# Performance work log

Hardware: AMD Instinct MI355X
Metric: run time of the kernel (lower is better)

The kernel has to match this reference:

```python
import jax, jax.numpy as jnp
import numpy as np

EPS = 1e-9  # Dice BatchNormalization epsilon


def dice(x, alpha):
    # Keras BatchNormalization(axis=-1, center=False, scale=False) in training
    # mode: normalize over all axes except the last using batch statistics.
    mean = jnp.mean(x, axis=(0, 1), keepdims=True)
    var = jnp.var(x, axis=(0, 1), keepdims=True)
    x_normed = (x - mean) * jax.lax.rsqrt(var + EPS)
    p = jax.nn.sigmoid(x_normed)
    return alpha * (1.0 - p) * x + p * x


def setup_inputs() -> dict:
    key = jax.random.key(0)
    ks = jax.random.split(key, 11)
    B, T, D = 512, 2048, 20
    keys_ = jax.random.normal(ks[0], (B, T, D), dtype=jnp.float32)
    query = jax.random.normal(ks[1], (B, 1, D), dtype=jnp.float32)
    mask = jax.random.randint(ks[2], (B, T), 0, 2) > 0
    # DNN tower weights: hidden dims 80 -> 32 -> 16, attention head 16 -> 1
    W0 = jax.random.normal(ks[3], (80, 32), dtype=jnp.float32) * 0.1
    b0 = jax.random.normal(ks[4], (32,), dtype=jnp.float32) * 0.1
    a0 = jax.random.normal(ks[5], (32,), dtype=jnp.float32) * 0.1
    W1 = jax.random.normal(ks[6], (32, 16), dtype=jnp.float32) * 0.1
    b1 = jax.random.normal(ks[7], (16,), dtype=jnp.float32) * 0.1
    a1 = jax.random.normal(ks[8], (16,), dtype=jnp.float32) * 0.1
    wk = jax.random.normal(ks[9], (16, 1), dtype=jnp.float32) * 0.1
    bk = jax.random.normal(ks[10], (1,), dtype=jnp.float32) * 0.1
    return {"keys": keys_, "query": query, "mask": mask,
            "W0": W0, "b0": b0, "a0": a0,
            "W1": W1, "b1": b1, "a1": a1,
            "wk": wk, "bk": bk}


def reference(keys, query, mask, W0, b0, a0, W1, b1, a1, wk, bk):
    B, T, D = keys.shape
    # repeat query along the key/time axis: [B,1,D] -> [B,T,D]
    queries = jnp.broadcast_to(query, (B, T, D))
    # local-activation features: [B,T,4D] = [B,T,80]
    att = jnp.concatenate([queries, keys, queries - keys, queries * keys], axis=-1)
    # DNN tower with Dice activations (dropout is identity at inference)
    h = dice(att @ W0 + b0, a0)   # [B,T,32]
    h = dice(h @ W1 + b1, a1)     # [B,T,16]
    score = h @ wk + bk           # [B,T,1]
    outputs = jnp.transpose(score, (0, 2, 1))  # [B,1,T]
    # NOTE: the original code computes the masked scores into self.outputs but
    # then (weight_normalization=False, return_score=False) overwrites it with
    # matmul(outputs, keys) using the UNMASKED scores -- we reproduce that.
    return jnp.matmul(outputs, keys)  # [B,1,D]
```

## Files before the change

### kernel.cpp

```cpp
#include <hip/hip_runtime.h>


#define BB 512
#define TT 2048
#define DD 20
#define C0 32
#define C1 16

#define NTH 256
#define NPOS 4
#define POSB (NTH * NPOS)

#define WS_SUM0 0
#define WS_SQ0 32
#define WS_SUM1 64
#define WS_SQ1 80
#define WS_BLOB 192
#define BLOB_J 24
#define BLOB_B (C0 * BLOB_J)
#define EPS 1e-9f

#define PIN(x) asm volatile("" : "+v"(x))

__device__ __forceinline__ float fast_sigmoid(float x) {
    return __builtin_amdgcn_rcpf(1.0f + __expf(-x));
}

__device__ __forceinline__ void load_krow(const float* __restrict__ row,
                                          float* kk) {
    const float4* kr = (const float4*)row;
    float4 a = kr[0], b = kr[1], c = kr[2], d = kr[3], e = kr[4];
    kk[0] = a.x; kk[1] = a.y; kk[2] = a.z; kk[3] = a.w;
    kk[4] = b.x; kk[5] = b.y; kk[6] = b.z; kk[7] = b.w;
    kk[8] = c.x; kk[9] = c.y; kk[10] = c.z; kk[11] = c.w;
    kk[12] = d.x; kk[13] = d.y; kk[14] = d.z; kk[15] = d.w;
    kk[16] = e.x; kk[17] = e.y; kk[18] = e.z; kk[19] = e.w;
}

__global__ void prep_kernel(const float* __restrict__ query,
                            const float* __restrict__ W0,
                            const float* __restrict__ b0,
                            float* __restrict__ blob) {
    const int b = blockIdx.x * 2 + (threadIdx.x >> 5);
    const int j = threadIdx.x & 31;
    float cj = b0[j];
    float* dst = blob + (size_t)b * BLOB_B + j * BLOB_J;
#pragma unroll
    for (int d = 0; d < DD; ++d) {
        float w_q = W0[d * C0 + j];
        float w_k = W0[(DD + d) * C0 + j];
        float w_d = W0[(2 * DD + d) * C0 + j];
        float w_p = W0[(3 * DD + d) * C0 + j];
        float qd = query[b * DD + d];
        dst[d] = w_k - w_d + qd * w_p;
        cj = fmaf(qd, w_q + w_d, cj);
    }
    dst[20] = cj;
}

__global__ __launch_bounds__(NTH, 2) void pass1_kernel(
    const float* __restrict__ keys, const float* __restrict__ blob,
    float* __restrict__ ws) {
    const int b = blockIdx.x >> 2, chunk = blockIdx.x & 3;
    const int tid = threadIdx.x, wave = tid >> 6, lane = tid & 63;
    const float* kbase = keys + ((size_t)b * TT + chunk * (TT / 4)) * DD;
    const float* wb = blob + (size_t)b * BLOB_B;

    float kk[2][DD];
    load_krow(kbase + (size_t)tid * DD, kk[0]);
    load_krow(kbase + (size_t)(tid + NTH) * DD, kk[1]);
#pragma unroll
    for (int pp = 0; pp < 2; ++pp)
#pragma unroll
        for (int d = 0; d < DD; ++d) PIN(kk[pp][d]);

    float s[C0], q[C0];
#pragma unroll
    for (int j = 0; j < C0; ++j) { s[j] = 0.f; q[j] = 0.f; }

#pragma unroll
    for (int j = 0; j < C0; ++j) {
        const float* w = wb + j * BLOB_J;
        float h0 = w[20], h1v = w[20];
#pragma unroll
        for (int d = 0; d < DD; ++d) {
            h0 = fmaf(kk[0][d], w[d], h0);
            h1v = fmaf(kk[1][d], w[d], h1v);
        }
        s[j] += h0 + h1v;
        q[j] = fmaf(h0, h0, q[j]);
        q[j] = fmaf(h1v, h1v, q[j]);
    }
    float mine = 0.f;
#pragma unroll
    for (int v = 0; v < 64; ++v) {
        float val = (v < C0) ? s[v] : q[v - C0];
#pragma unroll
        for (int o = 32; o >= 1; o >>= 1) val += __shfl_xor(val, o);
        if (lane == v) mine = val;
    }
    __shared__ float red[4][64];
    red[wave][lane] = mine;
    __syncthreads();
    if (tid < 64)
        atomicAdd(&ws[tid],
                  red[0][tid] + red[1][tid] + red[2][tid] + red[3][tid]);
}

#define LOAD_AND_PIN_KEYS()                                                  \
    const float* kbase = keys + ((size_t)b * TT + chunk * POSB) * DD;        \
    float kk[NPOS][DD];                                                      \
    _Pragma("unroll") for (int pp = 0; pp < NPOS; ++pp)                      \
        load_krow(kbase + (size_t)(tid + pp * NTH) * DD, kk[pp]);            \
    _Pragma("unroll") for (int pp = 0; pp < NPOS; ++pp)                      \
        _Pragma("unroll") for (int d = 0; d < DD; ++d) PIN(kk[pp][d]);

#define TOWER_JLOOP()                                                        \
    _Pragma("unroll 2") for (int j = 0; j < C0; ++j) {                       \
        float4 P = ld0[j];            \
        const float* w = wb + j * BLOB_J;             \
        const float* u = W1 + j * C1;                 \
        float h[NPOS];                                                       \
        _Pragma("unroll") for (int pp = 0; pp < NPOS; ++pp) {                \
            float hh = P.x;                                                  \
            _Pragma("unroll") for (int d = 0; d < DD; ++d)                   \
                hh = fmaf(kk[pp][d], w[d], hh);                              \
            h[pp] = hh;                                                      \
        }                                                                    \
        _Pragma("unroll") for (int pp = 0; pp < NPOS; ++pp) {                \
            float pr = fast_sigmoid(fmaf(h[pp], P.y, P.z));                  \
            float h0d = h[pp] * (P.w + pr * (1.0f - P.w));                   \
            _Pragma("unroll") for (int c = 0; c < C1; ++c)                   \
                h1[pp][c] = fmaf(h0d, u[c], h1[pp][c]);                      \
        }                                                                    \
    }

#define STAGE_DICE0()                                                        \
    if (tid < C0) {                                                          \
        const float invN = 1.0f / (float)(BB * TT);                          \
        float mean = ws[WS_SUM0 + tid] * invN;                               \
        float ex2 = ws[WS_SQ0 + tid] * invN;                                 \
        float sc = rsqrtf(ex2 - mean * mean + EPS);                          \
        ld0[tid] = make_float4(blob[(size_t)b * BLOB_B + tid * BLOB_J + 20], \
                               sc, -mean * sc, a0[tid]);                     \
    }

__global__ __launch_bounds__(NTH, 2) void pass2_kernel(
    const float* __restrict__ keys, const float* __restrict__ blob,
    const float* __restrict__ a0, const float* __restrict__ W1,
    const float* __restrict__ b1, float* __restrict__ ws) {
    const int b = blockIdx.x >> 1, chunk = blockIdx.x & 1;
    const int tid = threadIdx.x, wave = tid >> 6, lane = tid & 63;
    const float* wb = blob + (size_t)b * BLOB_B;
    __shared__ float4 ld0[C0];
    __shared__ float red[4][32];
    STAGE_DICE0()
    __syncthreads();

    LOAD_AND_PIN_KEYS()

    float h1[NPOS][C1];
#pragma unroll
    for (int pp = 0; pp < NPOS; ++pp)
#pragma unroll
        for (int c = 0; c < C1; ++c) h1[pp][c] = 0.f;

    TOWER_JLOOP()

    float s1[C1], q1[C1];
#pragma unroll
    for (int c = 0; c < C1; ++c) {
        float bc = b1[c], sv = 0.f, qv = 0.f;
#pragma unroll
        for (int pp = 0; pp < NPOS; ++pp) {
            float v = h1[pp][c] + bc;
            sv += v;
            qv = fmaf(v, v, qv);
        }
        s1[c] = sv;
        q1[c] = qv;
    }
    float mine = 0.f;
#pragma unroll
    for (int v = 0; v < 32; ++v) {
        float val = (v < C1) ? s1[v] : q1[v - C1];
#pragma unroll
        for (int o = 32; o >= 1; o >>= 1) val += __shfl_xor(val, o);
        if (lane == v) mine = val;
    }
    if (lane < 32) red[wave][lane] = mine;
    __syncthreads();
    if (tid < 32)
        atomicAdd(&ws[WS_SUM1 + tid],
                  red[0][tid] + red[1][tid] + red[2][tid] + red[3][tid]);
}

__global__ __launch_bounds__(NTH, 2) void pass3_kernel(
    const float* __restrict__ keys, const float* __restrict__ blob,
    const float* __restrict__ a0, const float* __restrict__ W1,
    const float* __restrict__ b1, const float* __restrict__ a1,
    const float* __restrict__ wk, const float* __restrict__ bk,
    const float* __restrict__ ws, float* __restrict__ out) {
    const int b = blockIdx.x >> 1, chunk = blockIdx.x & 1;
    const int tid = threadIdx.x, wave = tid >> 6, lane = tid & 63;
    const float* wb = blob + (size_t)b * BLOB_B;
    __shared__ float4 ld0[C0];
    __shared__ float4 ld1[C1];
    __shared__ float red[4][DD];
    STAGE_DICE0()
    if (tid < C1) {
        const float invN = 1.0f / (float)(BB * TT);
        float mean = ws[WS_SUM1 + tid] * invN;
        float ex2 = ws[WS_SQ1 + tid] * invN;
        float sc = rsqrtf(ex2 - mean * mean + EPS);
        ld1[tid] = make_float4(sc, -mean * sc, a1[tid], wk[tid]);
    }
    __syncthreads();

    LOAD_AND_PIN_KEYS()

    float h1[NPOS][C1];
#pragma unroll
    for (int pp = 0; pp < NPOS; ++pp)
#pragma unroll
        for (int c = 0; c < C1; ++c) h1[pp][c] = 0.f;

    TOWER_JLOOP()

    const float bkv = bk[0];
    float oacc[DD];
#pragma unroll
    for (int d = 0; d < DD; ++d) oacc[d] = 0.f;
#pragma unroll
    for (int pp = 0; pp < NPOS; ++pp) {
        float score = bkv;
#pragma unroll
        for (int c = 0; c < C1; ++c) {
            float v = h1[pp][c] + b1[c];
            float4 Q = ld1[c];
            float pr = fast_sigmoid(fmaf(v, Q.x, Q.y));
            float hd = v * (Q.z + pr * (1.0f - Q.z));
            score = fmaf(hd, Q.w, score);
        }
#pragma unroll
        for (int d = 0; d < DD; ++d) oacc[d] = fmaf(score, kk[pp][d], oacc[d]);
    }
    float mine = 0.f;
#pragma unroll
    for (int v = 0; v < DD; ++v) {
        float val = oacc[v];
#pragma unroll
        for (int o = 32; o >= 1; o >>= 1) val += __shfl_xor(val, o);
        if (lane == v) mine = val;
    }
    if (lane < DD) red[wave][lane] = mine;
    __syncthreads();
    if (tid < DD)
        atomicAdd(&out[b * DD + tid],
                  red[0][tid] + red[1][tid] + red[2][tid] + red[3][tid]);
}

extern "C" void kernel_launch(void* const* d_in, const int* in_sizes, int n_in,
                              void* d_out, int out_size, void* d_ws,
                              size_t ws_size, hipStream_t stream) {
    const float* keys = (const float*)d_in[0];
    const float* query = (const float*)d_in[1];
    const float* W0 = (const float*)d_in[3];
    const float* b0 = (const float*)d_in[4];
    const float* a0 = (const float*)d_in[5];
    const float* W1 = (const float*)d_in[6];
    const float* b1 = (const float*)d_in[7];
    const float* a1 = (const float*)d_in[8];
    const float* wk = (const float*)d_in[9];
    const float* bk = (const float*)d_in[10];
    float* out = (float*)d_out;
    float* ws = (float*)d_ws;
    float* blob = ws + WS_BLOB;

    hipMemsetAsync(ws, 0, 96 * sizeof(float), stream);
    hipMemsetAsync(out, 0, (size_t)out_size * sizeof(float), stream);

    prep_kernel<<<BB / 2, 64, 0, stream>>>(query, W0, b0, blob);

    pass1_kernel<<<BB * 4, NTH, 0, stream>>>(keys, blob, ws);
    pass2_kernel<<<BB * 2, NTH, 0, stream>>>(keys, blob, a0, W1, b1, ws);
    pass3_kernel<<<BB * 2, NTH, 0, stream>>>(keys, blob, a0, W1, b1, a1, wk,
                                             bk, ws, out);
}
```

Before: 298.5 us.

## Use reduce-scatter warp reductions, loop pass1 per batch, fully unroll tower

Replaces the per-value butterfly reductions (one full xor-shuffle tree per output value) with a reduce-scatter pattern that halves the live values at each shuffle stage, cutting the shuffle count in all three passes. Pass1 now launches one block per batch row and loops over the T axis in 4-row chunks instead of four blocks each handling two rows per thread, so each block does fewer atomics but the grid has fewer, longer blocks. The tower j-loop is fully unrolled and the Dice blend is rewritten as an fma. The trade-off is higher register pressure from the 64-entry value arrays and full unrolling, plus lower parallelism in pass1.

```diff
diff --git a/kernel.cpp b/kernel.cpp
--- a/kernel.cpp
+++ b/kernel.cpp
@@ -37,6 +37,36 @@
     kk[16] = e.x; kk[17] = e.y; kk[18] = e.z; kk[19] = e.w;
 }
 
+__device__ __forceinline__ float reduce_scatter_64(float* vals, int lane) {
+#pragma unroll
+    for (int m = 32; m >= 1; m >>= 1) {
+        bool hi = (lane & m) != 0;
+#pragma unroll
+        for (int i = 0; i < m; ++i) {
+            float keep = hi ? vals[m + i] : vals[i];
+            float send = hi ? vals[i] : vals[m + i];
+            vals[i] = keep + __shfl_xor(send, m);
+        }
+    }
+    return vals[0];
+}
+
+__device__ __forceinline__ float reduce_scatter_32(float* vals, int lane) {
+#pragma unroll
+    for (int i = 0; i < 32; ++i) vals[i] += __shfl_xor(vals[i], 32);
+#pragma unroll
+    for (int m = 16; m >= 1; m >>= 1) {
+        bool hi = (lane & m) != 0;
+#pragma unroll
+        for (int i = 0; i < m; ++i) {
+            float keep = hi ? vals[m + i] : vals[i];
+            float send = hi ? vals[i] : vals[m + i];
+            vals[i] = keep + __shfl_xor(send, m);
+        }
+    }
+    return vals[0];
+}
+
 __global__ void prep_kernel(const float* __restrict__ query,
                             const float* __restrict__ W0,
                             const float* __restrict__ b0,
@@ -61,46 +91,50 @@
 __global__ __launch_bounds__(NTH, 2) void pass1_kernel(
     const float* __restrict__ keys, const float* __restrict__ blob,
     float* __restrict__ ws) {
-    const int b = blockIdx.x >> 2, chunk = blockIdx.x & 3;
+    const int b = blockIdx.x;
     const int tid = threadIdx.x, wave = tid >> 6, lane = tid & 63;
-    const float* kbase = keys + ((size_t)b * TT + chunk * (TT / 4)) * DD;
+    const float* kbase = keys + (size_t)b * TT * DD;
     const float* wb = blob + (size_t)b * BLOB_B;
 
-    float kk[2][DD];
-    load_krow(kbase + (size_t)tid * DD, kk[0]);
-    load_krow(kbase + (size_t)(tid + NTH) * DD, kk[1]);
-#pragma unroll
-    for (int pp = 0; pp < 2; ++pp)
-#pragma unroll
-        for (int d = 0; d < DD; ++d) PIN(kk[pp][d]);
-
     float s[C0], q[C0];
 #pragma unroll
     for (int j = 0; j < C0; ++j) { s[j] = 0.f; q[j] = 0.f; }
 
-#pragma unroll
-    for (int j = 0; j < C0; ++j) {
-        const float* w = wb + j * BLOB_J;
-        float h0 = w[20], h1v = w[20];
-#pragma unroll
-        for (int d = 0; d < DD; ++d) {
-            h0 = fmaf(kk[0][d], w[d], h0);
-            h1v = fmaf(kk[1][d], w[d], h1v);
-        }
-        s[j] += h0 + h1v;
-        q[j] = fmaf(h0, h0, q[j]);
-        q[j] = fmaf(h1v, h1v, q[j]);
-    }
-    float mine = 0.f;
-#pragma unroll
-    for (int v = 0; v < 64; ++v) {
-        float val = (v < C0) ? s[v] : q[v - C0];
-#pragma unroll
-        for (int o = 32; o >= 1; o >>= 1) val += __shfl_xor(val, o);
-        if (lane == v) mine = val;
-    }
+#pragma unroll 1
+    for (int it = 0; it < TT / POSB; ++it) {
+        float kk[NPOS][DD];
+#pragma unroll
+        for (int pp = 0; pp < NPOS; ++pp)
+            load_krow(kbase + (size_t)(it * POSB + pp * NTH + tid) * DD,
+                      kk[pp]);
+#pragma unroll
+        for (int pp = 0; pp < NPOS; ++pp)
+#pragma unroll
+            for (int d = 0; d < DD; ++d) PIN(kk[pp][d]);
+
+#pragma unroll
+        for (int j = 0; j < C0; ++j) {
+            const float* w = wb + j * BLOB_J;
+            float h[NPOS];
+#pragma unroll
+            for (int pp = 0; pp < NPOS; ++pp) {
+                float hh = w[20];
+#pragma unroll
+                for (int d = 0; d < DD; ++d) hh = fmaf(kk[pp][d], w[d], hh);
+                h[pp] = hh;
+            }
+            s[j] += (h[0] + h[1]) + (h[2] + h[3]);
+#pragma unroll
+            for (int pp = 0; pp < NPOS; ++pp) q[j] = fmaf(h[pp], h[pp], q[j]);
+        }
+    }
+
+    float vals[64];
+#pragma unroll
+    for (int v = 0; v < 64; ++v) vals[v] = (v < C0) ? s[v] : q[v - C0];
+    float tot = reduce_scatter_64(vals, lane);
     __shared__ float red[4][64];
-    red[wave][lane] = mine;
+    red[wave][lane] = tot;
     __syncthreads();
     if (tid < 64)
         atomicAdd(&ws[tid],
@@ -116,7 +150,7 @@
         _Pragma("unroll") for (int d = 0; d < DD; ++d) PIN(kk[pp][d]);
 
 #define TOWER_JLOOP()                                                        \
-    _Pragma("unroll 2") for (int j = 0; j < C0; ++j) {                       \
+    _Pragma("unroll") for (int j = 0; j < C0; ++j) {                         \
         float4 P = ld0[j];            \
         const float* w = wb + j * BLOB_J;             \
         const float* u = W1 + j * C1;                 \
@@ -127,9 +161,10 @@
                 hh = fmaf(kk[pp][d], w[d], hh);                              \
             h[pp] = hh;                                                      \
         }                                                                    \
+        float oml = 1.0f - P.w;                                              \
         _Pragma("unroll") for (int pp = 0; pp < NPOS; ++pp) {                \
             float pr = fast_sigmoid(fmaf(h[pp], P.y, P.z));                  \
-            float h0d = h[pp] * (P.w + pr * (1.0f - P.w));                   \
+            float h0d = h[pp] * fmaf(pr, oml, P.w);                          \
             _Pragma("unroll") for (int c = 0; c < C1; ++c)                   \
                 h1[pp][c] = fmaf(h0d, u[c], h1[pp][c]);                      \
         }                                                                    \
@@ -167,7 +202,7 @@
 
     TOWER_JLOOP()
 
-    float s1[C1], q1[C1];
+    float vals[32];
 #pragma unroll
     for (int c = 0; c < C1; ++c) {
         float bc = b1[c], sv = 0.f, qv = 0.f;
@@ -177,18 +212,11 @@
             sv += v;
             qv = fmaf(v, v, qv);
         }
-        s1[c] = sv;
-        q1[c] = qv;
-    }
-    float mine = 0.f;
-#pragma unroll
-    for (int v = 0; v < 32; ++v) {
-        float val = (v < C1) ? s1[v] : q1[v - C1];
-#pragma unroll
-        for (int o = 32; o >= 1; o >>= 1) val += __shfl_xor(val, o);
-        if (lane == v) mine = val;
-    }
-    if (lane < 32) red[wave][lane] = mine;
+        vals[c] = sv;
+        vals[C1 + c] = qv;
+    }
+    float tot = reduce_scatter_32(vals, lane);
+    if (lane < 32) red[wave][lane] = tot;
     __syncthreads();
     if (tid < 32)
         atomicAdd(&ws[WS_SUM1 + tid],
@@ -206,7 +234,7 @@
     const float* wb = blob + (size_t)b * BLOB_B;
     __shared__ float4 ld0[C0];
     __shared__ float4 ld1[C1];
-    __shared__ float red[4][DD];
+    __shared__ float red[4][32];
     STAGE_DICE0()
     if (tid < C1) {
         const float invN = 1.0f / (float)(BB * TT);
@@ -239,21 +267,17 @@
             float v = h1[pp][c] + b1[c];
             float4 Q = ld1[c];
             float pr = fast_sigmoid(fmaf(v, Q.x, Q.y));
-            float hd = v * (Q.z + pr * (1.0f - Q.z));
+            float hd = v * fmaf(pr, 1.0f - Q.z, Q.z);
             score = fmaf(hd, Q.w, score);
         }
 #pragma unroll
         for (int d = 0; d < DD; ++d) oacc[d] = fmaf(score, kk[pp][d], oacc[d]);
     }
-    float mine = 0.f;
-#pragma unroll
-    for (int v = 0; v < DD; ++v) {
-        float val = oacc[v];
-#pragma unroll
-        for (int o = 32; o >= 1; o >>= 1) val += __shfl_xor(val, o);
-        if (lane == v) mine = val;
-    }
-    if (lane < DD) red[wave][lane] = mine;
+    float vals[32];
+#pragma unroll
+    for (int v = 0; v < 32; ++v) vals[v] = (v < DD) ? oacc[v] : 0.f;
+    float tot = reduce_scatter_32(vals, lane);
+    if (lane < 32) red[wave][lane] = tot;
     __syncthreads();
     if (tid < DD)
         atomicAdd(&out[b * DD + tid],
@@ -282,7 +306,7 @@
 
     prep_kernel<<<BB / 2, 64, 0, stream>>>(query, W0, b0, blob);
 
-    pass1_kernel<<<BB * 4, NTH, 0, stream>>>(keys, blob, ws);
+    pass1_kernel<<<BB, NTH, 0, stream>>>(keys, blob, ws);
     pass2_kernel<<<BB * 2, NTH, 0, stream>>>(keys, blob, a0, W1, b1, ws);
     pass3_kernel<<<BB * 2, NTH, 0, stream>>>(keys, blob, a0, W1, b1, a1, wk,
                                              bk, ws, out);
```

Result: slower. 349.4 us (+17.0%).
